# Performance work log

Measured on AMD Instinct MI355X. Metric: run time of the kernel, lower is better.

The kernel has to match this reference:

```python
import jax, jax.numpy as jnp
import numpy as np

N = 100000
E = 1600000
IN_CH, H1, H2 = 128, 128, 64


def gcn_conv(x, edge_index, W, b):
    """PyG GCNConv: add self-loops, symmetric normalization, linear + scatter-add."""
    n = x.shape[0]
    row, col = edge_index[0], edge_index[1]
    loop = jnp.arange(n, dtype=edge_index.dtype)
    row = jnp.concatenate([row, loop])  # sources (incl. self loops)
    col = jnp.concatenate([col, loop])  # targets
    h = x @ W                           # [n, out]
    deg = jax.ops.segment_sum(jnp.ones(row.shape[0], dtype=x.dtype), col, num_segments=n)
    dinv = jnp.where(deg > 0, jax.lax.rsqrt(deg), jnp.zeros((), dtype=x.dtype))
    norm = dinv[row] * dinv[col]        # [E+n]
    out = jax.ops.segment_sum(norm[:, None] * h[row], col, num_segments=n)
    return out + b


def setup_inputs() -> dict:
    key = jax.random.key(0)
    ks = jax.random.split(key, 8)
    x = jax.random.normal(ks[0], (N, IN_CH), dtype=jnp.float32)
    edge_index = jax.random.randint(ks[1], (2, E), 0, N, dtype=jnp.int32)
    batch = jnp.zeros((N,), dtype=jnp.int32)
    W1 = jax.random.normal(ks[2], (IN_CH, H1), dtype=jnp.float32) * 0.05
    b1 = jnp.zeros((H1,), dtype=jnp.float32)
    Wmu = jax.random.normal(ks[3], (H1, H2), dtype=jnp.float32) * 0.05
    bmu = jnp.zeros((H2,), dtype=jnp.float32)
    Wls = jax.random.normal(ks[4], (H1, H2), dtype=jnp.float32) * 0.05
    bls = jnp.zeros((H2,), dtype=jnp.float32)
    return {"x": x, "edge_index": edge_index, "batch": batch,
            "W1": W1, "b1": b1, "Wmu": Wmu, "bmu": bmu, "Wls": Wls, "bls": bls}


def reference(x, edge_index, batch, W1, b1, Wmu, bmu, Wls, bls):
    # classifier is None (use_classify=False), dropout=0 -> pure GCN path
    h = jax.nn.relu(gcn_conv(x, edge_index, W1, b1))
    mu = gcn_conv(h, edge_index, Wmu, bmu)
    logstd = gcn_conv(h, edge_index, Wls, bls)
    return (mu, logstd)
```

## Files before the change

### kernel.cpp

```cpp
#include <hip/hip_runtime.h>
#include <hip/hip_bf16.h>


#define BW_SH   8
#define BW      (1 << BW_SH)
#define NBUCK_MAX 512
#define EPB     6144
#define CAP     5120
#define GPAD    16

typedef __attribute__((ext_vector_type(8))) short bf16x8;
typedef __attribute__((ext_vector_type(4))) float f32x4;

__device__ __forceinline__ unsigned bf16rne(float f) {
    unsigned u = __float_as_uint(f);
    return (u + 0x7fffu + ((u >> 16) & 1u)) >> 16;
}
__device__ __forceinline__ float bflo(unsigned u) { return __uint_as_float(u << 16); }
__device__ __forceinline__ float bfhi(unsigned u) { return __uint_as_float(u & 0xffff0000u); }

__global__ void k_wprep(const float* __restrict__ W1,
                        const float* __restrict__ Wmu, const float* __restrict__ Wls,
                        const float* __restrict__ bmu, const float* __restrict__ bls,
                        unsigned short* __restrict__ W1t,
                        unsigned short* __restrict__ Wct,
                        float* __restrict__ bcat,
                        int* __restrict__ gcur, int nbuck) {
    int b = blockIdx.x, t = threadIdx.x;
    if (b < 128) {
        W1t[b * 128 + t] = (unsigned short)bf16rne(W1[t * 128 + b]);
        if (b == 0) bcat[t] = (t < 64) ? bmu[t] : bls[t - 64];
    } else if (b < 256) {
        int c = b - 128;
        float w = (c < 64) ? Wmu[t * 64 + c] : Wls[t * 64 + (c - 64)];
        Wct[c * 128 + t] = (unsigned short)bf16rne(w);
    } else {
        int idx = (b - 256) * 128 + t;
        if (idx < nbuck) gcur[idx * GPAD] = idx * CAP;
    }
}

__global__ __launch_bounds__(256) void k_bg1(
    const int* __restrict__ row, const int* __restrict__ col, int e,
    int* __restrict__ gcur, int* __restrict__ pairs,
    const float* __restrict__ X, const unsigned short* __restrict__ W1t,
    unsigned* __restrict__ Hbf, int n, int nbb)
{
    extern __shared__ char dsm[];
    int tid = threadIdx.x;
    if (blockIdx.x < nbb) {
        int* items = (int*)dsm;
        unsigned short* bkt = (unsigned short*)(dsm + 24576);
        int* hcnt  = (int*)(dsm + 24576 + 12288);
        int* lbase = hcnt + NBUCK_MAX;
        int e0 = blockIdx.x * EPB;
        int e1 = min(e, e0 + EPB);
        int m = e1 - e0;
        for (int b = tid; b < NBUCK_MAX; b += 256) hcnt[b] = 0;
        __syncthreads();
        for (int i = tid; i < m; i += 256) {
            int s = row[e0 + i];
            int d = col[e0 + i];
            items[i] = (s << BW_SH) | (d & (BW - 1));
            int b = d >> BW_SH;
            bkt[i] = (unsigned short)b;
            atomicAdd(&hcnt[b], 1);
        }
        __syncthreads();
        for (int b = tid; b < NBUCK_MAX; b += 256)
            lbase[b] = hcnt[b] ? atomicAdd(&gcur[b * GPAD], hcnt[b]) : 0;
        __syncthreads();
        for (int i = tid; i < m; i += 256) {
            int pos = atomicAdd(&lbase[bkt[i]], 1);
            pairs[pos] = items[i];
        }
    } else {
        unsigned short* ot = (unsigned short*)dsm;
        int w = tid >> 6, L = tid & 63;
        int q = L >> 4, ml = L & 15;
        int nb0 = (blockIdx.x - nbb) * 64 + w * 16;
        int node = nb0 + ml;
        bool valid = node < n;
        const bf16x8* Bp = (const bf16x8*)W1t;
        f32x4 acc[8];
        #pragma unroll
        for (int cb = 0; cb < 8; ++cb) { acc[cb][0]=0.f; acc[cb][1]=0.f; acc[cb][2]=0.f; acc[cb][3]=0.f; }
        #pragma unroll
        for (int kc = 0; kc < 4; ++kc) {
            bf16x8 af = {0,0,0,0,0,0,0,0};
            if (valid) {
                const float4* xp = (const float4*)&X[(size_t)node * 128 + kc * 32 + q * 8];
                float4 xa = xp[0], xb = xp[1];
                af[0] = (short)bf16rne(xa.x); af[1] = (short)bf16rne(xa.y);
                af[2] = (short)bf16rne(xa.z); af[3] = (short)bf16rne(xa.w);
                af[4] = (short)bf16rne(xb.x); af[5] = (short)bf16rne(xb.y);
                af[6] = (short)bf16rne(xb.z); af[7] = (short)bf16rne(xb.w);
            }
            #pragma unroll
            for (int cb = 0; cb < 8; ++cb) {
                bf16x8 bfr = Bp[(cb * 16 + ml) * 16 + kc * 4 + q];
                acc[cb] = __builtin_amdgcn_mfma_f32_16x16x32_bf16(af, bfr, acc[cb], 0, 0, 0);
            }
        }
        #pragma unroll
        for (int cb = 0; cb < 8; ++cb)
            #pragma unroll
            for (int r = 0; r < 4; ++r)
                ot[(w * 16 + q * 4 + r) * 136 + cb * 16 + ml] =
                    (unsigned short)bf16rne(acc[cb][r]);
        __syncthreads();
        #pragma unroll
        for (int it = 0; it < 4; ++it) {
            int flat = it * 64 + L;
            int rw = flat >> 4, cg = flat & 15;
            int nd = nb0 + rw;
            if (nd < n) {
                uint4 v = *(const uint4*)&ot[(w * 16 + rw) * 136 + cg * 8];
                *(uint4*)&Hbf[(size_t)nd * 64 + cg * 4] = v;
            }
        }
    }
}

__global__ __launch_bounds__(256) void k_fill5(
    const int* __restrict__ gcur, const int* __restrict__ pairs,
    int* __restrict__ offs, int* __restrict__ cnt, float* __restrict__ dinv,
    int* __restrict__ esrc, int n)
{
    __shared__ int lcnt[BW];
    __shared__ int loffs[BW];
    __shared__ int lcur[BW];
    __shared__ int sscan[256];
    __shared__ int lesrc[CAP];
    int b = blockIdx.x, tid = threadIdx.x;
    int t0 = b << BW_SH;
    int nt = min(n - t0, BW);
    int base = b * CAP;
    int m = min(gcur[b * GPAD] - base, CAP);
    lcnt[tid] = 0;
    __syncthreads();
    for (int i = tid; i < m; i += 256)
        atomicAdd(&lcnt[pairs[base + i] & (BW - 1)], 1);
    __syncthreads();
    int s = lcnt[tid];
    sscan[tid] = s; __syncthreads();
    for (int d = 1; d < 256; d <<= 1) {
        int u = (tid >= d) ? sscan[tid - d] : 0;
        __syncthreads();
        sscan[tid] += u;
        __syncthreads();
    }
    int ex = sscan[tid] - s;
    loffs[tid] = ex; lcur[tid] = ex;
    __syncthreads();
    if (tid < nt) {
        offs[t0 + tid] = base + ex;
        cnt[t0 + tid]  = s;
        dinv[t0 + tid] = 1.0f / sqrtf((float)(s + 1));
    }
    for (int i = tid; i < m; i += 256) {
        int it = pairs[base + i];
        int pos = atomicAdd(&lcur[it & (BW - 1)], 1);
        lesrc[pos] = it >> BW_SH;
    }
    __syncthreads();
    for (int i = tid; i < m; i += 256)
        esrc[base + i] = lesrc[i];
}

__global__ __launch_bounds__(256) void k_prop_bf(
    const unsigned* __restrict__ hbf, const float* __restrict__ dinv,
    const int* __restrict__ offs, const int* __restrict__ cnt,
    const int* __restrict__ esrc,
    unsigned* __restrict__ out_bf,
    const float* __restrict__ bias, int do_relu, int n)
{
    int wid  = (blockIdx.x * blockDim.x + threadIdx.x) >> 6;
    if (wid >= n) return;
    int lane = threadIdx.x & 63;
    int half = lane >> 5;
    int fl   = lane & 31;
    int v = wid;
    float dv = dinv[v];
    int start = offs[v];
    int deg   = cnt[v];
    const uint2* rows = (const uint2*)hbf;

    float a0 = 0.f, a1 = 0.f, a2 = 0.f, a3 = 0.f;
    if (half == 0) {
        uint2 r = rows[(size_t)v * 32 + fl];
        a0 = dv * bflo(r.x); a1 = dv * bfhi(r.x);
        a2 = dv * bflo(r.y); a3 = dv * bfhi(r.y);
    }
    for (int base = 0; base < deg; base += 64) {
        int m = min(64, deg - base);
        int s = 0; float w = 0.f;
        if (lane < m) { s = esrc[start + base + lane]; w = dinv[s]; }
        int j = 0;
        for (; j + 16 <= m; j += 16) {
            int si[8]; float wi[8]; uint2 r[8];
            #pragma unroll
            for (int u = 0; u < 8; ++u) {
                si[u] = __shfl(s, j + 2 * u + half);
                wi[u] = __shfl(w, j + 2 * u + half);
            }
            #pragma unroll
            for (int u = 0; u < 8; ++u) r[u] = rows[(size_t)si[u] * 32 + fl];
            #pragma unroll
            for (int u = 0; u < 8; ++u) {
                a0 = fmaf(wi[u], bflo(r[u].x), a0);
                a1 = fmaf(wi[u], bfhi(r[u].x), a1);
                a2 = fmaf(wi[u], bflo(r[u].y), a2);
                a3 = fmaf(wi[u], bfhi(r[u].y), a3);
            }
        }
        for (; j + 8 <= m; j += 8) {
            int si[4]; float wi[4]; uint2 r[4];
            #pragma unroll
            for (int u = 0; u < 4; ++u) {
                si[u] = __shfl(s, j + 2 * u + half);
                wi[u] = __shfl(w, j + 2 * u + half);
            }
            #pragma unroll
            for (int u = 0; u < 4; ++u) r[u] = rows[(size_t)si[u] * 32 + fl];
            #pragma unroll
            for (int u = 0; u < 4; ++u) {
                a0 = fmaf(wi[u], bflo(r[u].x), a0);
                a1 = fmaf(wi[u], bfhi(r[u].x), a1);
                a2 = fmaf(wi[u], bflo(r[u].y), a2);
                a3 = fmaf(wi[u], bfhi(r[u].y), a3);
            }
        }
        for (; j < m; j += 2) {
            int   ss = __shfl(s, j + half);
            float wv = __shfl(w, j + half);
            uint2 r = rows[(size_t)ss * 32 + fl];
            a0 = fmaf(wv, bflo(r.x), a0); a1 = fmaf(wv, bfhi(r.x), a1);
            a2 = fmaf(wv, bflo(r.y), a2); a3 = fmaf(wv, bfhi(r.y), a3);
        }
    }
    a0 += __shfl_xor(a0, 32);
    a1 += __shfl_xor(a1, 32);
    a2 += __shfl_xor(a2, 32);
    a3 += __shfl_xor(a3, 32);
    if (half == 0) {
        a0 *= dv; a1 *= dv; a2 *= dv; a3 *= dv;
        if (bias) {
            a0 += bias[fl * 4 + 0]; a1 += bias[fl * 4 + 1];
            a2 += bias[fl * 4 + 2]; a3 += bias[fl * 4 + 3];
        }
        if (do_relu) {
            a0 = fmaxf(a0, 0.f); a1 = fmaxf(a1, 0.f);
            a2 = fmaxf(a2, 0.f); a3 = fmaxf(a3, 0.f);
        }
        uint2 pk;
        pk.x = (bf16rne(a1) << 16) | bf16rne(a0);
        pk.y = (bf16rne(a3) << 16) | bf16rne(a2);
        ((uint2*)out_bf)[(size_t)v * 32 + fl] = pk;
    }
}

__global__ __launch_bounds__(256) void k_gemm2(
    const unsigned* __restrict__ Gbf, const unsigned short* __restrict__ Wct,
    const float* __restrict__ bcat, float* __restrict__ out, int n)
{
    __shared__ float ot[4][16][132];
    int tid = threadIdx.x;
    int w = tid >> 6, L = tid & 63;
    int q = L >> 4, ml = L & 15;
    int nb0 = blockIdx.x * 64 + w * 16;
    int node = nb0 + ml;
    bool valid = node < n;
    const bf16x8* Ap = (const bf16x8*)Gbf;
    const bf16x8* Bp = (const bf16x8*)Wct;
    f32x4 acc[8];
    #pragma unroll
    for (int cb = 0; cb < 8; ++cb) { acc[cb][0]=0.f; acc[cb][1]=0.f; acc[cb][2]=0.f; acc[cb][3]=0.f; }
    #pragma unroll
    for (int kc = 0; kc < 4; ++kc) {
        bf16x8 af = {0,0,0,0,0,0,0,0};
        if (valid) af = Ap[(size_t)node * 16 + kc * 4 + q];
        #pragma unroll
        for (int cb = 0; cb < 8; ++cb) {
            bf16x8 bfr = Bp[(cb * 16 + ml) * 16 + kc * 4 + q];
            acc[cb] = __builtin_amdgcn_mfma_f32_16x16x32_bf16(af, bfr, acc[cb], 0, 0, 0);
        }
    }
    #pragma unroll
    for (int cb = 0; cb < 8; ++cb)
        #pragma unroll
        for (int r = 0; r < 4; ++r)
            ot[w][q * 4 + r][cb * 16 + ml] = acc[cb][r];
    __syncthreads();
    #pragma unroll
    for (int it = 0; it < 8; ++it) {
        int flat = it * 64 + L;
        int row = flat >> 5, c4 = flat & 31;
        int col = c4 * 4;
        int nd = nb0 + row;
        if (nd < n) {
            float4 v = *(const float4*)&ot[w][row][col];
            float4 bb = *(const float4*)&bcat[col];
            v.x += bb.x; v.y += bb.y; v.z += bb.z; v.w += bb.w;
            size_t off = (col < 64)
                ? ((size_t)nd * 64 + col)
                : ((size_t)n * 64 + (size_t)nd * 64 + (col - 64));
            *(float4*)&out[off] = v;
        }
    }
}

extern "C" void kernel_launch(void* const* d_in, const int* in_sizes, int n_in,
                              void* d_out, int out_size, void* d_ws, size_t ws_size,
                              hipStream_t stream) {
    const float* x   = (const float*)d_in[0];
    const int*   ei  = (const int*)d_in[1];
    const float* W1  = (const float*)d_in[3];
    const float* b1  = (const float*)d_in[4];
    const float* Wmu = (const float*)d_in[5];
    const float* bmu = (const float*)d_in[6];
    const float* Wls = (const float*)d_in[7];
    const float* bls = (const float*)d_in[8];
    float* out = (float*)d_out;

    int n = in_sizes[0] / 128;
    int e = in_sizes[1] / 2;
    const int* erow = ei;
    const int* ecol = ei + e;
    int nbuck = (n + BW - 1) >> BW_SH;
    int nbb   = (e + EPB - 1) / EPB;

    char* p = (char*)d_ws;
    auto alloc = [&](size_t bytes) -> char* {
        char* q = p; p += (bytes + 255) & ~(size_t)255; return q;
    };
    int*            gcur  = (int*)           alloc((size_t)NBUCK_MAX * GPAD * 4);
    int*            cnt   = (int*)           alloc((size_t)n * 4);
    int*            offs  = (int*)           alloc((size_t)n * 4);
    float*          dinv  = (float*)         alloc((size_t)n * 4);
    int*            esrc  = (int*)           alloc((size_t)nbuck * CAP * 4);
    unsigned short* W1t   = (unsigned short*)alloc(128 * 128 * 2);
    unsigned short* Wct   = (unsigned short*)alloc(128 * 128 * 2);
    float*          bcat  = (float*)         alloc(128 * 4);
    unsigned*       hbf   = (unsigned*)      alloc((size_t)n * 64 * 4);
    unsigned*       h1bf  = (unsigned*)      alloc((size_t)n * 64 * 4);
    unsigned*       gbf   = (unsigned*)      alloc((size_t)n * 64 * 4);
    int*            pairs = (int*)gbf;

    k_wprep<<<260, 128, 0, stream>>>(W1, Wmu, Wls, bmu, bls, W1t, Wct, bcat,
                                     gcur, nbuck);
    k_bg1<<<nbb + (n + 63) / 64, 256, 40960, stream>>>(
        erow, ecol, e, gcur, pairs, x, W1t, hbf, n, nbb);
    k_fill5<<<nbuck, 256, 0, stream>>>(gcur, pairs, offs, cnt, dinv, esrc, n);

    k_prop_bf<<<(n + 3) / 4, 256, 0, stream>>>(hbf, dinv, offs, cnt, esrc,
                                               h1bf, b1, 1, n);
    k_prop_bf<<<(n + 3) / 4, 256, 0, stream>>>(h1bf, dinv, offs, cnt, esrc,
                                               gbf, nullptr, 0, n);
    k_gemm2<<<(n + 63) / 64, 256, 0, stream>>>(gbf, Wct, bcat, out, n);
}
```

Before: 321.1 us.

## Slice feature matrix into column groups and propagate each slice per block

```diff
diff --git a/kernel.cpp b/kernel.cpp
--- a/kernel.cpp
+++ b/kernel.cpp
@@ -8,6 +8,8 @@
 #define EPB     6144
 #define CAP     5120
 #define GPAD    16
+#define NSL     8
+#define SLC     16
 
 typedef __attribute__((ext_vector_type(8))) short bf16x8;
 typedef __attribute__((ext_vector_type(4))) float f32x4;
@@ -116,7 +118,7 @@
             int nd = nb0 + rw;
             if (nd < n) {
                 uint4 v = *(const uint4*)&ot[(w * 16 + rw) * 136 + cg * 8];
-                *(uint4*)&Hbf[(size_t)nd * 64 + cg * 4] = v;
+                *(uint4*)&Hbf[((size_t)(cg >> 1) * n + nd) * 8 + (cg & 1) * 4] = v;
             }
         }
     }
@@ -168,95 +170,85 @@
         esrc[base + i] = lesrc[i];
 }
 
-__global__ __launch_bounds__(256) void k_prop_bf(
-    const unsigned* __restrict__ hbf, const float* __restrict__ dinv,
+__global__ __launch_bounds__(256) void k_prop_sg(
+    const unsigned* __restrict__ hin, const float* __restrict__ dinv,
     const int* __restrict__ offs, const int* __restrict__ cnt,
     const int* __restrict__ esrc,
-    unsigned* __restrict__ out_bf,
-    const float* __restrict__ bias, int do_relu, int n)
+    unsigned* __restrict__ hout, const float* __restrict__ bias,
+    int do_relu, int n)
 {
-    int wid  = (blockIdx.x * blockDim.x + threadIdx.x) >> 6;
-    if (wid >= n) return;
-    int lane = threadIdx.x & 63;
-    int half = lane >> 5;
-    int fl   = lane & 31;
-    int v = wid;
-    float dv = dinv[v];
-    int start = offs[v];
-    int deg   = cnt[v];
-    const uint2* rows = (const uint2*)hbf;
-
-    float a0 = 0.f, a1 = 0.f, a2 = 0.f, a3 = 0.f;
-    if (half == 0) {
-        uint2 r = rows[(size_t)v * 32 + fl];
-        a0 = dv * bflo(r.x); a1 = dv * bfhi(r.x);
-        a2 = dv * bflo(r.y); a3 = dv * bfhi(r.y);
-    }
-    for (int base = 0; base < deg; base += 64) {
-        int m = min(64, deg - base);
-        int s = 0; float w = 0.f;
-        if (lane < m) { s = esrc[start + base + lane]; w = dinv[s]; }
-        int j = 0;
-        for (; j + 16 <= m; j += 16) {
-            int si[8]; float wi[8]; uint2 r[8];
-            #pragma unroll
-            for (int u = 0; u < 8; ++u) {
-                si[u] = __shfl(s, j + 2 * u + half);
-                wi[u] = __shfl(w, j + 2 * u + half);
-            }
-            #pragma unroll
-            for (int u = 0; u < 8; ++u) r[u] = rows[(size_t)si[u] * 32 + fl];
-            #pragma unroll
-            for (int u = 0; u < 8; ++u) {
-                a0 = fmaf(wi[u], bflo(r[u].x), a0);
-                a1 = fmaf(wi[u], bfhi(r[u].x), a1);
-                a2 = fmaf(wi[u], bflo(r[u].y), a2);
-                a3 = fmaf(wi[u], bfhi(r[u].y), a3);
-            }
-        }
-        for (; j + 8 <= m; j += 8) {
-            int si[4]; float wi[4]; uint2 r[4];
-            #pragma unroll
-            for (int u = 0; u < 4; ++u) {
-                si[u] = __shfl(s, j + 2 * u + half);
-                wi[u] = __shfl(w, j + 2 * u + half);
-            }
-            #pragma unroll
-            for (int u = 0; u < 4; ++u) r[u] = rows[(size_t)si[u] * 32 + fl];
-            #pragma unroll
-            for (int u = 0; u < 4; ++u) {
-                a0 = fmaf(wi[u], bflo(r[u].x), a0);
-                a1 = fmaf(wi[u], bfhi(r[u].x), a1);
-                a2 = fmaf(wi[u], bflo(r[u].y), a2);
-                a3 = fmaf(wi[u], bfhi(r[u].y), a3);
-            }
-        }
-        for (; j < m; j += 2) {
-            int   ss = __shfl(s, j + half);
-            float wv = __shfl(w, j + half);
-            uint2 r = rows[(size_t)ss * 32 + fl];
-            a0 = fmaf(wv, bflo(r.x), a0); a1 = fmaf(wv, bfhi(r.x), a1);
-            a2 = fmaf(wv, bflo(r.y), a2); a3 = fmaf(wv, bfhi(r.y), a3);
-        }
-    }
-    a0 += __shfl_xor(a0, 32);
-    a1 += __shfl_xor(a1, 32);
-    a2 += __shfl_xor(a2, 32);
-    a3 += __shfl_xor(a3, 32);
-    if (half == 0) {
-        a0 *= dv; a1 *= dv; a2 *= dv; a3 *= dv;
-        if (bias) {
-            a0 += bias[fl * 4 + 0]; a1 += bias[fl * 4 + 1];
-            a2 += bias[fl * 4 + 2]; a3 += bias[fl * 4 + 3];
-        }
-        if (do_relu) {
-            a0 = fmaxf(a0, 0.f); a1 = fmaxf(a1, 0.f);
-            a2 = fmaxf(a2, 0.f); a3 = fmaxf(a3, 0.f);
-        }
-        uint2 pk;
-        pk.x = (bf16rne(a1) << 16) | bf16rne(a0);
-        pk.y = (bf16rne(a3) << 16) | bf16rne(a2);
-        ((uint2*)out_bf)[(size_t)v * 32 + fl] = pk;
+    int b   = blockIdx.x >> 3;
+    int g   = blockIdx.x & 7;
+    int tid = threadIdx.x;
+    int w   = tid >> 6, lane = tid & 63;
+    int t0  = (b << BW_SH) + w * 64;
+
+    int  myn    = t0 + lane;
+    bool nvalid = myn < n;
+    int   startv = nvalid ? offs[myn] : 0;
+    int   degv   = nvalid ? cnt[myn]  : 0;
+    float dvv    = nvalid ? dinv[myn] : 0.f;
+
+    const uint2* rows    = (const uint2*)(hin  + (size_t)g * n * 8);
+    uint2*       outrows = (uint2*)      (hout + (size_t)g * n * 8);
+
+    int fl  = lane & 3;
+    int ep  = (lane >> 2) & 3;
+    int sub = lane >> 4;
+
+    for (int gi = 0; gi < 16; ++gi) {
+        int nidx  = gi * 4 + sub;
+        int start = __shfl(startv, nidx);
+        int deg   = __shfl(degv,   nidx);
+        float dv  = __shfl(dvv,    nidx);
+        int node  = t0 + nidx;
+
+        float a0 = 0.f, a1 = 0.f, a2 = 0.f, a3 = 0.f;
+        int e = ep;
+        for (; e + 4 < deg; e += 8) {
+            int s0 = __builtin_nontemporal_load(&esrc[start + e]);
+            int s1 = __builtin_nontemporal_load(&esrc[start + e + 4]);
+            float w0 = dinv[s0];
+            float w1 = dinv[s1];
+            uint2 r0 = rows[(unsigned)(s0 * 4 + fl)];
+            uint2 r1 = rows[(unsigned)(s1 * 4 + fl)];
+            a0 = fmaf(w0, bflo(r0.x), a0); a1 = fmaf(w0, bfhi(r0.x), a1);
+            a2 = fmaf(w0, bflo(r0.y), a2); a3 = fmaf(w0, bfhi(r0.y), a3);
+            a0 = fmaf(w1, bflo(r1.x), a0); a1 = fmaf(w1, bfhi(r1.x), a1);
+            a2 = fmaf(w1, bflo(r1.y), a2); a3 = fmaf(w1, bfhi(r1.y), a3);
+        }
+        if (e < deg) {
+            int s0 = __builtin_nontemporal_load(&esrc[start + e]);
+            float w0 = dinv[s0];
+            uint2 r0 = rows[(unsigned)(s0 * 4 + fl)];
+            a0 = fmaf(w0, bflo(r0.x), a0); a1 = fmaf(w0, bfhi(r0.x), a1);
+            a2 = fmaf(w0, bflo(r0.y), a2); a3 = fmaf(w0, bfhi(r0.y), a3);
+        }
+        a0 += __shfl_xor(a0, 4); a0 += __shfl_xor(a0, 8);
+        a1 += __shfl_xor(a1, 4); a1 += __shfl_xor(a1, 8);
+        a2 += __shfl_xor(a2, 4); a2 += __shfl_xor(a2, 8);
+        a3 += __shfl_xor(a3, 4); a3 += __shfl_xor(a3, 8);
+
+        if (ep == 0 && node < n) {
+            uint2 rs = rows[(unsigned)(node * 4 + fl)];
+            float c0 = a0 + dv * bflo(rs.x);
+            float c1 = a1 + dv * bfhi(rs.x);
+            float c2 = a2 + dv * bflo(rs.y);
+            float c3 = a3 + dv * bfhi(rs.y);
+            c0 *= dv; c1 *= dv; c2 *= dv; c3 *= dv;
+            if (bias) {
+                const float* bp = &bias[g * SLC + fl * 4];
+                c0 += bp[0]; c1 += bp[1]; c2 += bp[2]; c3 += bp[3];
+            }
+            if (do_relu) {
+                c0 = fmaxf(c0, 0.f); c1 = fmaxf(c1, 0.f);
+                c2 = fmaxf(c2, 0.f); c3 = fmaxf(c3, 0.f);
+            }
+            uint2 pk;
+            pk.x = (bf16rne(c1) << 16) | bf16rne(c0);
+            pk.y = (bf16rne(c3) << 16) | bf16rne(c2);
+            outrows[(unsigned)(node * 4 + fl)] = pk;
+        }
     }
 }
 
@@ -279,7 +271,10 @@
     #pragma unroll
     for (int kc = 0; kc < 4; ++kc) {
         bf16x8 af = {0,0,0,0,0,0,0,0};
-        if (valid) af = Ap[(size_t)node * 16 + kc * 4 + q];
+        if (valid) {
+            int cc = kc * 4 + q;
+            af = Ap[((size_t)(cc >> 1) * n + node) * 2 + (cc & 1)];
+        }
         #pragma unroll
         for (int cb = 0; cb < 8; ++cb) {
             bf16x8 bfr = Bp[(cb * 16 + ml) * 16 + kc * 4 + q];
@@ -353,9 +348,9 @@
         erow, ecol, e, gcur, pairs, x, W1t, hbf, n, nbb);
     k_fill5<<<nbuck, 256, 0, stream>>>(gcur, pairs, offs, cnt, dinv, esrc, n);
 
-    k_prop_bf<<<(n + 3) / 4, 256, 0, stream>>>(hbf, dinv, offs, cnt, esrc,
+    k_prop_sg<<<nbuck * NSL, 256, 0, stream>>>(hbf, dinv, offs, cnt, esrc,
                                                h1bf, b1, 1, n);
-    k_prop_bf<<<(n + 3) / 4, 256, 0, stream>>>(h1bf, dinv, offs, cnt, esrc,
+    k_prop_sg<<<nbuck * NSL, 256, 0, stream>>>(h1bf, dinv, offs, cnt, esrc,
                                                gbf, nullptr, 0, n);
     k_gemm2<<<(n + 63) / 64, 256, 0, stream>>>(gbf, Wct, bcat, out, n);
 }
```

New measurement: 633.1 us. 1.97x slower.

## Process two nodes per wave in propagation, wave-shuffle scan, nontemporal output stores

Applied to the files above, without the earlier changes.

```diff
diff --git a/kernel.cpp b/kernel.cpp
--- a/kernel.cpp
+++ b/kernel.cpp
@@ -128,9 +128,8 @@
     int* __restrict__ esrc, int n)
 {
     __shared__ int lcnt[BW];
-    __shared__ int loffs[BW];
     __shared__ int lcur[BW];
-    __shared__ int sscan[256];
+    __shared__ int wsum[4];
     __shared__ int lesrc[CAP];
     int b = blockIdx.x, tid = threadIdx.x;
     int t0 = b << BW_SH;
@@ -143,15 +142,20 @@
         atomicAdd(&lcnt[pairs[base + i] & (BW - 1)], 1);
     __syncthreads();
     int s = lcnt[tid];
-    sscan[tid] = s; __syncthreads();
-    for (int d = 1; d < 256; d <<= 1) {
-        int u = (tid >= d) ? sscan[tid - d] : 0;
-        __syncthreads();
-        sscan[tid] += u;
-        __syncthreads();
-    }
-    int ex = sscan[tid] - s;
-    loffs[tid] = ex; lcur[tid] = ex;
+    int x = s;
+    #pragma unroll
+    for (int d = 1; d < 64; d <<= 1) {
+        int t = __shfl_up(x, d);
+        if ((tid & 63) >= d) x += t;
+    }
+    if ((tid & 63) == 63) wsum[tid >> 6] = x;
+    __syncthreads();
+    int pre = 0;
+    #pragma unroll
+    for (int i = 0; i < 4; ++i)
+        if (i < (tid >> 6)) pre += wsum[i];
+    int ex = pre + x - s;
+    lcur[tid] = ex;
     __syncthreads();
     if (tid < nt) {
         offs[t0 + tid] = base + ex;
@@ -168,95 +172,98 @@
         esrc[base + i] = lesrc[i];
 }
 
-__global__ __launch_bounds__(256) void k_prop_bf(
+__global__ __launch_bounds__(256) void k_prop_bf2(
     const unsigned* __restrict__ hbf, const float* __restrict__ dinv,
     const int* __restrict__ offs, const int* __restrict__ cnt,
     const int* __restrict__ esrc,
     unsigned* __restrict__ out_bf,
     const float* __restrict__ bias, int do_relu, int n)
 {
-    int wid  = (blockIdx.x * blockDim.x + threadIdx.x) >> 6;
-    if (wid >= n) return;
+    int wid = (blockIdx.x * blockDim.x + threadIdx.x) >> 6;
+    int v0  = wid * 2;
+    if (v0 >= n) return;
+    int v1  = v0 + 1;
+    bool hasB = v1 < n;
     int lane = threadIdx.x & 63;
     int half = lane >> 5;
     int fl   = lane & 31;
-    int v = wid;
-    float dv = dinv[v];
-    int start = offs[v];
-    int deg   = cnt[v];
     const uint2* rows = (const uint2*)hbf;
 
-    float a0 = 0.f, a1 = 0.f, a2 = 0.f, a3 = 0.f;
+    float dvA = dinv[v0];
+    int   stA = offs[v0], dgA = cnt[v0];
+    float dvB = hasB ? dinv[v1] : 0.f;
+    int   stB = hasB ? offs[v1] : 0;
+    int   dgB = hasB ? cnt[v1]  : 0;
+
+    float aA0=0.f,aA1=0.f,aA2=0.f,aA3=0.f;
+    float aB0=0.f,aB1=0.f,aB2=0.f,aB3=0.f;
     if (half == 0) {
-        uint2 r = rows[(size_t)v * 32 + fl];
-        a0 = dv * bflo(r.x); a1 = dv * bfhi(r.x);
-        a2 = dv * bflo(r.y); a3 = dv * bfhi(r.y);
-    }
-    for (int base = 0; base < deg; base += 64) {
-        int m = min(64, deg - base);
-        int s = 0; float w = 0.f;
-        if (lane < m) { s = esrc[start + base + lane]; w = dinv[s]; }
-        int j = 0;
-        for (; j + 16 <= m; j += 16) {
-            int si[8]; float wi[8]; uint2 r[8];
-            #pragma unroll
-            for (int u = 0; u < 8; ++u) {
-                si[u] = __shfl(s, j + 2 * u + half);
-                wi[u] = __shfl(w, j + 2 * u + half);
-            }
-            #pragma unroll
-            for (int u = 0; u < 8; ++u) r[u] = rows[(size_t)si[u] * 32 + fl];
-            #pragma unroll
-            for (int u = 0; u < 8; ++u) {
-                a0 = fmaf(wi[u], bflo(r[u].x), a0);
-                a1 = fmaf(wi[u], bfhi(r[u].x), a1);
-                a2 = fmaf(wi[u], bflo(r[u].y), a2);
-                a3 = fmaf(wi[u], bfhi(r[u].y), a3);
-            }
-        }
-        for (; j + 8 <= m; j += 8) {
-            int si[4]; float wi[4]; uint2 r[4];
+        uint2 r = rows[(size_t)v0 * 32 + fl];
+        aA0 = dvA * bflo(r.x); aA1 = dvA * bfhi(r.x);
+        aA2 = dvA * bflo(r.y); aA3 = dvA * bfhi(r.y);
+    } else if (hasB) {
+        uint2 r = rows[(size_t)v1 * 32 + fl];
+        aB0 = dvB * bflo(r.x); aB1 = dvB * bfhi(r.x);
+        aB2 = dvB * bflo(r.y); aB3 = dvB * bfhi(r.y);
+    }
+
+    int dmax = max(dgA, dgB);
+    for (int base = 0; base < dmax; base += 64) {
+        int mA = dgA - base;
+        int mB = dgB - base;
+        int sA = 0, sB = 0; float wA = 0.f, wB = 0.f;
+        if (lane < mA) { sA = esrc[stA + base + lane]; wA = dinv[sA]; }
+        if (lane < mB) { sB = esrc[stB + base + lane]; wB = dinv[sB]; }
+        int mm = min(max(mA, mB), 64);
+        for (int j = 0; j < mm; j += 8) {
+            int siA[4], siB[4]; float wiA[4], wiB[4]; uint2 rA[4], rB[4];
             #pragma unroll
             for (int u = 0; u < 4; ++u) {
-                si[u] = __shfl(s, j + 2 * u + half);
-                wi[u] = __shfl(w, j + 2 * u + half);
-            }
-            #pragma unroll
-            for (int u = 0; u < 4; ++u) r[u] = rows[(size_t)si[u] * 32 + fl];
+                siA[u] = __shfl(sA, j + 2 * u + half);
+                wiA[u] = __shfl(wA, j + 2 * u + half);
+                siB[u] = __shfl(sB, j + 2 * u + half);
+                wiB[u] = __shfl(wB, j + 2 * u + half);
+            }
             #pragma unroll
             for (int u = 0; u < 4; ++u) {
-                a0 = fmaf(wi[u], bflo(r[u].x), a0);
-                a1 = fmaf(wi[u], bfhi(r[u].x), a1);
-                a2 = fmaf(wi[u], bflo(r[u].y), a2);
-                a3 = fmaf(wi[u], bfhi(r[u].y), a3);
-            }
-        }
-        for (; j < m; j += 2) {
-            int   ss = __shfl(s, j + half);
-            float wv = __shfl(w, j + half);
-            uint2 r = rows[(size_t)ss * 32 + fl];
-            a0 = fmaf(wv, bflo(r.x), a0); a1 = fmaf(wv, bfhi(r.x), a1);
-            a2 = fmaf(wv, bflo(r.y), a2); a3 = fmaf(wv, bfhi(r.y), a3);
-        }
-    }
-    a0 += __shfl_xor(a0, 32);
-    a1 += __shfl_xor(a1, 32);
-    a2 += __shfl_xor(a2, 32);
-    a3 += __shfl_xor(a3, 32);
-    if (half == 0) {
-        a0 *= dv; a1 *= dv; a2 *= dv; a3 *= dv;
+                rA[u] = rows[(size_t)siA[u] * 32 + fl];
+                rB[u] = rows[(size_t)siB[u] * 32 + fl];
+            }
+            #pragma unroll
+            for (int u = 0; u < 4; ++u) {
+                aA0 = fmaf(wiA[u], bflo(rA[u].x), aA0);
+                aA1 = fmaf(wiA[u], bfhi(rA[u].x), aA1);
+                aA2 = fmaf(wiA[u], bflo(rA[u].y), aA2);
+                aA3 = fmaf(wiA[u], bfhi(rA[u].y), aA3);
+                aB0 = fmaf(wiB[u], bflo(rB[u].x), aB0);
+                aB1 = fmaf(wiB[u], bfhi(rB[u].x), aB1);
+                aB2 = fmaf(wiB[u], bflo(rB[u].y), aB2);
+                aB3 = fmaf(wiB[u], bfhi(rB[u].y), aB3);
+            }
+        }
+    }
+    aA0 += __shfl_xor(aA0, 32); aA1 += __shfl_xor(aA1, 32);
+    aA2 += __shfl_xor(aA2, 32); aA3 += __shfl_xor(aA3, 32);
+    aB0 += __shfl_xor(aB0, 32); aB1 += __shfl_xor(aB1, 32);
+    aB2 += __shfl_xor(aB2, 32); aB3 += __shfl_xor(aB3, 32);
+
+    float c0, c1, c2, c3, dv; int vout;
+    if (half == 0) { c0=aA0; c1=aA1; c2=aA2; c3=aA3; dv=dvA; vout=v0; }
+    else           { c0=aB0; c1=aB1; c2=aB2; c3=aB3; dv=dvB; vout=v1; }
+    if (half == 0 || hasB) {
+        c0 *= dv; c1 *= dv; c2 *= dv; c3 *= dv;
         if (bias) {
-            a0 += bias[fl * 4 + 0]; a1 += bias[fl * 4 + 1];
-            a2 += bias[fl * 4 + 2]; a3 += bias[fl * 4 + 3];
+            c0 += bias[fl * 4 + 0]; c1 += bias[fl * 4 + 1];
+            c2 += bias[fl * 4 + 2]; c3 += bias[fl * 4 + 3];
         }
         if (do_relu) {
-            a0 = fmaxf(a0, 0.f); a1 = fmaxf(a1, 0.f);
-            a2 = fmaxf(a2, 0.f); a3 = fmaxf(a3, 0.f);
+            c0 = fmaxf(c0, 0.f); c1 = fmaxf(c1, 0.f);
+            c2 = fmaxf(c2, 0.f); c3 = fmaxf(c3, 0.f);
         }
         uint2 pk;
-        pk.x = (bf16rne(a1) << 16) | bf16rne(a0);
-        pk.y = (bf16rne(a3) << 16) | bf16rne(a2);
-        ((uint2*)out_bf)[(size_t)v * 32 + fl] = pk;
+        pk.x = (bf16rne(c1) << 16) | bf16rne(c0);
+        pk.y = (bf16rne(c3) << 16) | bf16rne(c2);
+        ((uint2*)out_bf)[(size_t)vout * 32 + fl] = pk;
     }
 }
 
@@ -301,11 +308,13 @@
         if (nd < n) {
             float4 v = *(const float4*)&ot[w][row][col];
             float4 bb = *(const float4*)&bcat[col];
-            v.x += bb.x; v.y += bb.y; v.z += bb.z; v.w += bb.w;
+            f32x4 vv;
+            vv[0] = v.x + bb.x; vv[1] = v.y + bb.y;
+            vv[2] = v.z + bb.z; vv[3] = v.w + bb.w;
             size_t off = (col < 64)
                 ? ((size_t)nd * 64 + col)
                 : ((size_t)n * 64 + (size_t)nd * 64 + (col - 64));
-            *(float4*)&out[off] = v;
+            __builtin_nontemporal_store(vv, (f32x4*)&out[off]);
         }
     }
 }
@@ -353,9 +362,11 @@
         erow, ecol, e, gcur, pairs, x, W1t, hbf, n, nbb);
     k_fill5<<<nbuck, 256, 0, stream>>>(gcur, pairs, offs, cnt, dinv, esrc, n);
 
-    k_prop_bf<<<(n + 3) / 4, 256, 0, stream>>>(hbf, dinv, offs, cnt, esrc,
-                                               h1bf, b1, 1, n);
-    k_prop_bf<<<(n + 3) / 4, 256, 0, stream>>>(h1bf, dinv, offs, cnt, esrc,
-                                               gbf, nullptr, 0, n);
+    int nwaves = (n + 1) / 2;
+    int pblocks = (nwaves + 3) / 4;
+    k_prop_bf2<<<pblocks, 256, 0, stream>>>(hbf, dinv, offs, cnt, esrc,
+                                            h1bf, b1, 1, n);
+    k_prop_bf2<<<pblocks, 256, 0, stream>>>(h1bf, dinv, offs, cnt, esrc,
+                                            gbf, nullptr, 0, n);
     k_gemm2<<<(n + 63) / 64, 256, 0, stream>>>(gbf, Wct, bcat, out, n);
 }
```

Result: no change. 319.5 us (-0.5%).
